# Performance work log

Measured on AMD Instinct MI355X. Metric: run time of the kernel, lower is better.

The kernel has to match this reference:

```python
import jax, jax.numpy as jnp
import numpy as np

B, S, D, H, FF = 4, 2048, 512, 8, 2048
HD = D // H
SCALE = float(D) ** 0.5  # original scales by sqrt(embed_dim), not sqrt(head_dim)
EPS = 1e-5


def setup_inputs() -> dict:
    key = jax.random.key(0)
    ks = jax.random.split(key, 16)
    s_in = 1.0 / np.sqrt(D)
    s_ff = 1.0 / np.sqrt(FF)
    return {
        "embeddings": jax.random.normal(ks[0], (B, S, D), dtype=jnp.float32),
        "mask": jnp.ones((B, S), dtype=bool),
        # per-head Q/K/V projections stacked: [H, D, HD]
        "Wq": jax.random.uniform(ks[1], (H, D, HD), jnp.float32, -s_in, s_in),
        "bq": jax.random.uniform(ks[2], (H, HD), jnp.float32, -s_in, s_in),
        "Wk": jax.random.uniform(ks[3], (H, D, HD), jnp.float32, -s_in, s_in),
        "bk": jax.random.uniform(ks[4], (H, HD), jnp.float32, -s_in, s_in),
        "Wv": jax.random.uniform(ks[5], (H, D, HD), jnp.float32, -s_in, s_in),
        "bv": jax.random.uniform(ks[6], (H, HD), jnp.float32, -s_in, s_in),
        "Wc": jax.random.uniform(ks[7], (D, D), jnp.float32, -s_in, s_in),
        "bc": jax.random.uniform(ks[8], (D,), jnp.float32, -s_in, s_in),
        "W1": jax.random.uniform(ks[9], (D, FF), jnp.float32, -s_in, s_in),
        "b1": jax.random.uniform(ks[10], (FF,), jnp.float32, -s_in, s_in),
        "W2": jax.random.uniform(ks[11], (FF, D), jnp.float32, -s_ff, s_ff),
        "b2": jax.random.uniform(ks[12], (D,), jnp.float32, -s_ff, s_ff),
        "gamma": jnp.ones((D,), jnp.float32),
        "beta": jnp.zeros((D,), jnp.float32),
    }


def reference(embeddings, mask, Wq, bq, Wk, bk, Wv, bv, Wc, bc, W1, b1, W2, b2, gamma, beta):
    # Per-head projections batched into one einsum each: [B,H,S,HD]
    Q = jnp.einsum("bsd,hdf->bhsf", embeddings, Wq) + bq[:, None, :]
    K = jnp.einsum("bsd,hdf->bhsf", embeddings, Wk) + bk[:, None, :]
    V = jnp.einsum("bsd,hdf->bhsf", embeddings, Wv) + bv[:, None, :]
    # NOTE: the original computes a masked score tensor but then softmaxes the
    # UNMASKED scores (bug). We faithfully ignore the mask here.
    scores = jnp.einsum("bhsf,bhtf->bhst", Q, K) / SCALE  # [B,H,S,S]
    A = jax.nn.softmax(scores, axis=-1)
    Hh = jnp.einsum("bhst,bhtf->bhsf", A, V)  # [B,H,S,HD]
    # concat heads along feature dim (head h -> contiguous slice)
    Hcat = jnp.transpose(Hh, (0, 2, 1, 3)).reshape(B, S, D)
    Hp = Hcat @ Wc + bc
    # add & norm (dropout is identity at eval)
    res = Hp + embeddings
    mu = jnp.mean(res, axis=-1, keepdims=True)
    var = jnp.var(res, axis=-1, keepdims=True)
    Hn = (res - mu) / jnp.sqrt(var + EPS) * gamma + beta
    out = jax.nn.relu(Hn @ W1 + b1) @ W2 + b2  # no residual after FFN in original
    return out, mask
```

## Files before the change

kernel.cpp:

```cpp
#include <hip/hip_runtime.h>
#include <hip/hip_bf16.h>
#include <cstdint>
#include <cstddef>

typedef short  s16x8 __attribute__((ext_vector_type(8)));
typedef short  s16x4 __attribute__((ext_vector_type(4)));
typedef float  f32x4 __attribute__((ext_vector_type(4)));
typedef unsigned u32x2 __attribute__((ext_vector_type(2)));

static constexpr int Bb = 4, Ss = 2048, Dd = 512, Hh = 8, HDd = 64, FFf = 2048;
static constexpr int Mm = Bb * Ss;

__device__ __forceinline__ unsigned short f2bf(float f) {
  unsigned u = __float_as_uint(f);
  u += 0x7FFFu + ((u >> 16) & 1u);
  return (unsigned short)(u >> 16);
}

__device__ __forceinline__ unsigned cvt_pk_bf16(float lo, float hi) {
  unsigned r;
  asm("v_cvt_pk_bf16_f32 %0, %1, %2" : "=v"(r) : "v"(lo), "v"(hi));
  return r;
}

__device__ __forceinline__ float exp2_raw(float x) {
  float r;
  asm("v_exp_f32 %0, %1\n\ts_nop 0" : "=v"(r) : "v"(x));
  return r;
}

#define GLOAD_LDS16(gp, lp)                                                     \
  __builtin_amdgcn_global_load_lds((const __attribute__((address_space(1))) void*)(gp), \
                                   (__attribute__((address_space(3))) void*)(lp), 16, 0, 0)

__device__ __forceinline__ void xpose_tile(const float* __restrict__ in,
                                           unsigned short* __restrict__ out,
                                           int K, int N, int bx, int by, float (*t)[33]) {
  const int lx = threadIdx.x & 31, ly = threadIdx.x >> 5;
  const int n0 = bx * 32, k0 = by * 32;
#pragma unroll
  for (int r = 0; r < 4; ++r) t[ly + r * 8][lx] = in[(size_t)(k0 + ly + r * 8) * N + n0 + lx];
  __syncthreads();
#pragma unroll
  for (int r = 0; r < 4; ++r)
    out[(size_t)(n0 + ly + r * 8) * K + k0 + lx] = f2bf(t[lx][ly + r * 8]);
}

__global__ __launch_bounds__(256) void prep_all(
    const float* __restrict__ emb, const float* __restrict__ Wq, const float* __restrict__ Wk,
    const float* __restrict__ Wv, const float* __restrict__ Wc, const float* __restrict__ W1,
    const float* __restrict__ W2, unsigned short* __restrict__ embB,
    unsigned short* __restrict__ WtQKV, unsigned short* __restrict__ WtC,
    unsigned short* __restrict__ Wt1, unsigned short* __restrict__ Wt2,
    float* __restrict__ maskOut) {
  __shared__ float t[32][33];
  const int blk = blockIdx.x;
  if (blk < 4096) {
    const int i = blk * 256 + threadIdx.x;
    const float4 v = reinterpret_cast<const float4*>(emb)[i];
    s16x4 o; o[0] = f2bf(v.x); o[1] = f2bf(v.y); o[2] = f2bf(v.z); o[3] = f2bf(v.w);
    reinterpret_cast<s16x4*>(embB)[i] = o;
  } else if (blk < 4864) {
    const int b = blk - 4096;
    const int bx = b & 15, by = (b >> 4) & 1, z = b >> 5;
    const int sel = z >> 3, h = z & 7;
    const float* W = sel == 0 ? Wq : (sel == 1 ? Wk : Wv);
    const float* inb = W + (size_t)h * 512 * 64;
    unsigned short* outb = WtQKV + (size_t)sel * 512 * 512 + (size_t)h * 64 * 512;
    const int lx = threadIdx.x & 31, ly = threadIdx.x >> 5;
    const int d0 = bx * 32, f0 = by * 32;
#pragma unroll
    for (int r = 0; r < 4; ++r) t[ly + r * 8][lx] = inb[(size_t)(d0 + ly + r * 8) * 64 + f0 + lx];
    __syncthreads();
#pragma unroll
    for (int r = 0; r < 4; ++r)
      outb[(size_t)(f0 + ly + r * 8) * 512 + d0 + lx] = f2bf(t[lx][ly + r * 8]);
  } else if (blk < 5120) {
    const int b = blk - 4864;
    xpose_tile(Wc, WtC, 512, 512, b & 15, b >> 4, t);
  } else if (blk < 6144) {
    const int b = blk - 5120;
    xpose_tile(W1, Wt1, 512, 2048, b & 63, b >> 6, t);
  } else if (blk < 7168) {
    const int b = blk - 6144;
    xpose_tile(W2, Wt2, 2048, 512, b & 15, b >> 4, t);
  } else {
    const int i = (blk - 7168) * 256 + threadIdx.x;
    if (i < Bb * Ss) maskOut[i] = 1.0f;
  }
}

template<int EPI, int NI>
__global__ __launch_bounds__(256) void gemm_bt(
    const unsigned short* __restrict__ A, const unsigned short* __restrict__ Bt,
    const float* __restrict__ bias0, const float* __restrict__ bias1, const float* __restrict__ bias2,
    const float* __restrict__ addf, float* __restrict__ outF,
    unsigned short* __restrict__ outB0, unsigned short* __restrict__ outB1,
    unsigned short* __restrict__ outB2, int M, int N, int K, int nbx) {
  constexpr int BN = NI * 32;
  __shared__ alignas(16) unsigned short As[3][128 * 32];
  __shared__ alignas(16) unsigned short Bs[3][BN * 32];
  const int tid = threadIdx.x;
  const int lane = tid & 63, wid = tid >> 6;
  const int wr = wid >> 1, wc = wid & 1;
  const int fr = lane & 15, kg = lane >> 4;

  const int lin = blockIdx.x;
  const int xcd = lin & 7, idx = lin >> 3;
  const int bx = idx % nbx, ysub = idx / nbx;
  const int m0 = (xcd * 8 + ysub) * 128, n0 = bx * BN;

  const int srow = tid >> 2;
  const int schunk = (tid & 3) ^ ((tid >> 3) & 3);
  const unsigned short* gA = A + (size_t)(m0 + srow) * K + (schunk << 3);
  const unsigned short* gB = Bt + (size_t)(n0 + srow) * K + (schunk << 3);

  auto STAGE = [&](int kt, int buf) {
    unsigned short* lA = &As[buf][wid * 512];
    unsigned short* lB = &Bs[buf][wid * 512];
    GLOAD_LDS16(gA + kt, lA);
    GLOAD_LDS16(gA + (size_t)64 * K + kt, lA + 2048);
    GLOAD_LDS16(gB + kt, lB);
    if constexpr (NI == 4) GLOAD_LDS16(gB + (size_t)64 * K + kt, lB + 2048);
  };

  f32x4 acc[4][NI];
#pragma unroll
  for (int i = 0; i < 4; ++i)
#pragma unroll
    for (int j = 0; j < NI; ++j)
#pragma unroll
      for (int r = 0; r < 4; ++r) acc[i][j][r] = 0.f;

  STAGE(0, 0);
  STAGE(32, 1);
  const int nk = K >> 5;
  int cur = 0;
  const int rchunk = (kg ^ ((fr >> 1) & 3)) << 3;
  for (int ki = 0; ki < nk; ++ki) {
    const int pre = cur == 0 ? 2 : cur - 1;
    __builtin_amdgcn_s_barrier();
    if (ki + 2 < nk) {
      STAGE((ki + 2) << 5, pre);
      if constexpr (NI == 4)
        asm volatile("s_waitcnt vmcnt(8)" ::: "memory");
      else
        asm volatile("s_waitcnt vmcnt(6)" ::: "memory");
    } else if (ki + 1 < nk) {
      if constexpr (NI == 4)
        asm volatile("s_waitcnt vmcnt(4)" ::: "memory");
      else
        asm volatile("s_waitcnt vmcnt(3)" ::: "memory");
    } else {
      asm volatile("s_waitcnt vmcnt(0)" ::: "memory");
    }
    __builtin_amdgcn_sched_barrier(0);
    __builtin_amdgcn_s_barrier();
    __builtin_amdgcn_sched_barrier(0);

    s16x8 af[4], bfv[NI];
#pragma unroll
    for (int i = 0; i < 4; ++i)
      af[i] = *reinterpret_cast<const s16x8*>(&As[cur][(wr * 64 + i * 16 + fr) * 32 + rchunk]);
#pragma unroll
    for (int i = 0; i < NI; ++i)
      bfv[i] = *reinterpret_cast<const s16x8*>(
          &Bs[cur][(wc * (NI * 16) + i * 16 + fr) * 32 + rchunk]);
    __builtin_amdgcn_s_setprio(1);
#pragma unroll
    for (int mi = 0; mi < 4; ++mi)
#pragma unroll
      for (int ni = 0; ni < NI; ++ni)
        acc[mi][ni] = __builtin_amdgcn_mfma_f32_16x16x32_bf16(af[mi], bfv[ni], acc[mi][ni], 0, 0, 0);
    __builtin_amdgcn_s_setprio(0);
    cur = cur == 2 ? 0 : cur + 1;
  }

#pragma unroll
  for (int mi = 0; mi < 4; ++mi)
#pragma unroll
    for (int ni = 0; ni < NI; ++ni) {
      if constexpr (EPI == 0) {
        const int col = n0 + wc * (NI * 16) + ni * 16 + fr;
        const int sel = col >> 9, c = col & 511;
        const int h = c >> 6, f = c & 63;
        const int row0 = m0 + wr * 64 + mi * 16 + kg * 4;
        const int b = row0 >> 11, s0 = row0 & 2047;
        if (sel == 2) {
          const float bsv = bias2[c];
          u32x2 pk;
          pk[0] = (unsigned)f2bf(acc[mi][ni][0] + bsv) |
                  ((unsigned)f2bf(acc[mi][ni][1] + bsv) << 16);
          pk[1] = (unsigned)f2bf(acc[mi][ni][2] + bsv) |
                  ((unsigned)f2bf(acc[mi][ni][3] + bsv) << 16);
          *reinterpret_cast<u32x2*>(
              &outB2[((size_t)((b << 3) + h) * 64 + f) * 2048 + s0]) = pk;
        } else {
          const float* bs = sel == 0 ? bias0 : bias1;
          unsigned short* ob = sel == 0 ? outB0 : outB1;
          const float bv = bs[c];
#pragma unroll
          for (int r = 0; r < 4; ++r)
            ob[((size_t)((b << 3) + h) * 2048 + s0 + r) * 64 + f] =
                f2bf(acc[mi][ni][r] + bv);
        }
      } else {
#pragma unroll
        for (int r = 0; r < 4; ++r) {
          const int row = m0 + wr * 64 + mi * 16 + kg * 4 + r;
          const int col = n0 + wc * (NI * 16) + ni * 16 + fr;
          float v = acc[mi][ni][r];
          if constexpr (EPI == 1) {
            const size_t idx2 = (size_t)row * 512 + col;
            outF[idx2] = v + bias0[col] + addf[idx2];
          } else if constexpr (EPI == 2) {
            v += bias0[col];
            outB0[(size_t)row * 2048 + col] = f2bf(v > 0.f ? v : 0.f);
          } else {
            outF[(size_t)row * 512 + col] = v + bias0[col];
          }
        }
      }
    }
}

__global__ __launch_bounds__(512) void attn_kernel(const unsigned short* __restrict__ Q,
                                                   const unsigned short* __restrict__ Kx,
                                                   const unsigned short* __restrict__ V,
                                                   unsigned short* __restrict__ Hcat) {
  const int lane = threadIdx.x & 63, wid = threadIdx.x >> 6;
  const int fr = lane & 15, kg = lane >> 4;
  const int lin = blockIdx.x;
  const int xcd = lin & 7, idx = lin >> 3;
  const int bh = xcd * 4 + (idx & 3);
  const int qi = idx >> 2;
  const int b = bh >> 3, h = bh & 7;
  const int q0 = qi * 128 + wid * 16;
  const unsigned short* Qh = Q + (size_t)bh * Ss * HDd;
  const unsigned short* Kh = Kx + (size_t)bh * Ss * HDd;
  const unsigned short* Vh = V + (size_t)bh * HDd * Ss;

  __shared__ alignas(16) unsigned short Ks[2][64 * 64];
  __shared__ alignas(16) unsigned short Vs[64 * 64];
  __shared__ alignas(16) unsigned short P[8][16][72];

  const int srow = lane >> 3;
  const int scol = ((lane & 7) ^ srow) << 3;
  const unsigned short* gK = Kh + (size_t)(8 * wid + srow) * 64 + scol;
  const unsigned short* gV = Vh + (size_t)(8 * wid + srow) * 2048 + scol;
  unsigned short* lKa = &Ks[0][wid * 512];
  unsigned short* lKb = &Ks[1][wid * 512];
  unsigned short* lV  = &Vs[wid * 512];

  s16x8 bq[2];
#pragma unroll
  for (int kb = 0; kb < 2; ++kb)
    bq[kb] = *reinterpret_cast<const s16x8*>(&Qh[(size_t)(q0 + fr) * 64 + kb * 32 + kg * 8]);

  f32x4 o[4];
#pragma unroll
  for (int ct = 0; ct < 4; ++ct)
#pragma unroll
    for (int r = 0; r < 4; ++r) o[ct][r] = 0.f;
  float mr = -1e30f, lsum = 0.f;

  const float iscL = 1.4426950408889634f * 0.044194173824159216f;
  const int swz = (fr & 7) << 3;

  GLOAD_LDS16(gK, lKa);
  GLOAD_LDS16(gV, lV);

#pragma unroll 1
  for (int t = 0; t < 32; ++t) {
    const int kt = t * 64;
    const int ktn = (kt + 64) & 2047;
    const unsigned short* KsC = Ks[t & 1];
    unsigned short* nK = (t & 1) ? lKa : lKb;

    asm volatile("s_waitcnt vmcnt(1)" ::: "memory");
    __builtin_amdgcn_sched_barrier(0);
    __builtin_amdgcn_s_barrier();
    __builtin_amdgcn_sched_barrier(0);

    f32x4 sc[4];
#pragma unroll
    for (int ct = 0; ct < 4; ++ct)
#pragma unroll
      for (int r = 0; r < 4; ++r) sc[ct][r] = 0.f;
    __builtin_amdgcn_s_setprio(1);
#pragma unroll
    for (int ct = 0; ct < 4; ++ct)
#pragma unroll
      for (int kb = 0; kb < 2; ++kb) {
        const s16x8 kf = *reinterpret_cast<const s16x8*>(
            &KsC[(ct * 16 + fr) * 64 + (((kg << 3) + (kb << 5)) ^ swz)]);
        sc[ct] = __builtin_amdgcn_mfma_f32_16x16x32_bf16(kf, bq[kb], sc[ct], 0, 0, 0);
      }
    __builtin_amdgcn_s_setprio(0);

    GLOAD_LDS16(gK + (size_t)ktn * 64, nK);

    float mxl;
    {
      const float a0 = fmaxf(fmaxf(sc[0][0], sc[0][1]), fmaxf(sc[0][2], sc[0][3]));
      const float a1 = fmaxf(fmaxf(sc[1][0], sc[1][1]), fmaxf(sc[1][2], sc[1][3]));
      const float a2 = fmaxf(fmaxf(sc[2][0], sc[2][1]), fmaxf(sc[2][2], sc[2][3]));
      const float a3 = fmaxf(fmaxf(sc[3][0], sc[3][1]), fmaxf(sc[3][2], sc[3][3]));
      mxl = fmaxf(fmaxf(a0, a1), fmaxf(a2, a3)) * iscL;
    }
    if (!__all(mxl <= mr + 8.0f)) {
      float mx = fmaxf(mxl, __shfl_xor(mxl, 16));
      mx = fmaxf(mx, __shfl_xor(mx, 32));
      const float mn = fmaxf(mr, mx);
      const float corr = exp2_raw(mr - mn);
      mr = mn;
      lsum *= corr;
      float corrq[4];
#pragma unroll
      for (int r = 0; r < 4; ++r) corrq[r] = __shfl(corr, kg * 4 + r);
#pragma unroll
      for (int ct = 0; ct < 4; ++ct)
#pragma unroll
        for (int r = 0; r < 4; ++r) o[ct][r] *= corrq[r];
    }

    float ps0 = 0.f, ps1 = 0.f;
#pragma unroll
    for (int ct = 0; ct < 4; ++ct) {
      float p0 = exp2_raw(__builtin_fmaf(sc[ct][0], iscL, -mr));
      float p1 = exp2_raw(__builtin_fmaf(sc[ct][1], iscL, -mr));
      float p2 = exp2_raw(__builtin_fmaf(sc[ct][2], iscL, -mr));
      float p3 = exp2_raw(__builtin_fmaf(sc[ct][3], iscL, -mr));
      ps0 += (p0 + p1);
      ps1 += (p2 + p3);
      u32x2 pk;
      pk[0] = cvt_pk_bf16(p0, p1);
      pk[1] = cvt_pk_bf16(p2, p3);
      *reinterpret_cast<u32x2*>(&P[wid][fr][ct * 16 + kg * 4]) = pk;
    }
    lsum += ps0 + ps1;

    asm volatile("s_waitcnt vmcnt(1)" ::: "memory");
    __builtin_amdgcn_sched_barrier(0);
    __builtin_amdgcn_s_barrier();
    __builtin_amdgcn_sched_barrier(0);

    const s16x8 pa0 = *reinterpret_cast<const s16x8*>(&P[wid][fr][kg * 8]);
    const s16x8 pa1 = *reinterpret_cast<const s16x8*>(&P[wid][fr][32 + kg * 8]);
    __builtin_amdgcn_s_setprio(1);
#pragma unroll
    for (int ct = 0; ct < 4; ++ct) {
      const s16x8 bv0 = *reinterpret_cast<const s16x8*>(
          &Vs[(ct * 16 + fr) * 64 + (((kg << 3) + 0) ^ swz)]);
      o[ct] = __builtin_amdgcn_mfma_f32_16x16x32_bf16(pa0, bv0, o[ct], 0, 0, 0);
      const s16x8 bv1 = *reinterpret_cast<const s16x8*>(
          &Vs[(ct * 16 + fr) * 64 + (((kg << 3) + 32) ^ swz)]);
      o[ct] = __builtin_amdgcn_mfma_f32_16x16x32_bf16(pa1, bv1, o[ct], 0, 0, 0);
    }
    __builtin_amdgcn_s_setprio(0);

    __builtin_amdgcn_s_barrier();
    __builtin_amdgcn_sched_barrier(0);
    GLOAD_LDS16(gV + ktn, lV);
  }

  lsum += __shfl_xor(lsum, 16);
  lsum += __shfl_xor(lsum, 32);
  float invq[4];
#pragma unroll
  for (int r = 0; r < 4; ++r) invq[r] = 1.0f / __shfl(lsum, kg * 4 + r);
#pragma unroll
  for (int ct = 0; ct < 4; ++ct)
#pragma unroll
    for (int r = 0; r < 4; ++r) {
      const int qrow = q0 + kg * 4 + r;
      Hcat[(size_t)(b * Ss + qrow) * Dd + h * 64 + ct * 16 + fr] = f2bf(o[ct][r] * invq[r]);
    }
}

__global__ __launch_bounds__(256) void layernorm_k(const float* __restrict__ res,
                                                   const float* __restrict__ gamma,
                                                   const float* __restrict__ beta,
                                                   unsigned short* __restrict__ out) {
  const int lane = threadIdx.x & 63, wid = threadIdx.x >> 6;
  const int row = blockIdx.x * 4 + wid;
  const float* rp = res + (size_t)row * 512 + lane * 8;
  const float4 v0 = *reinterpret_cast<const float4*>(rp);
  const float4 v1 = *reinterpret_cast<const float4*>(rp + 4);
  float x[8] = {v0.x, v0.y, v0.z, v0.w, v1.x, v1.y, v1.z, v1.w};
  float s = 0.f, q = 0.f;
#pragma unroll
  for (int j = 0; j < 8; ++j) { s += x[j]; q += x[j] * x[j]; }
#pragma unroll
  for (int off = 32; off; off >>= 1) { s += __shfl_xor(s, off); q += __shfl_xor(q, off); }
  const float mean = s * (1.f / 512.f);
  const float var = q * (1.f / 512.f) - mean * mean;
  const float rstd = rsqrtf(var + 1e-5f);
  s16x8 o;
#pragma unroll
  for (int j = 0; j < 8; ++j) {
    const int c = lane * 8 + j;
    o[j] = f2bf((x[j] - mean) * rstd * gamma[c] + beta[c]);
  }
  *reinterpret_cast<s16x8*>(out + (size_t)row * 512 + lane * 8) = o;
}

extern "C" void kernel_launch(void* const* d_in, const int* in_sizes, int n_in,
                              void* d_out, int out_size, void* d_ws, size_t ws_size,
                              hipStream_t stream) {
  const float* emb = (const float*)d_in[0];
  const float* Wq = (const float*)d_in[2];
  const float* bq = (const float*)d_in[3];
  const float* Wk = (const float*)d_in[4];
  const float* bk = (const float*)d_in[5];
  const float* Wv = (const float*)d_in[6];
  const float* bv = (const float*)d_in[7];
  const float* Wc = (const float*)d_in[8];
  const float* bc = (const float*)d_in[9];
  const float* W1 = (const float*)d_in[10];
  const float* b1 = (const float*)d_in[11];
  const float* W2 = (const float*)d_in[12];
  const float* b2 = (const float*)d_in[13];
  const float* gamma = (const float*)d_in[14];
  const float* beta = (const float*)d_in[15];
  float* out = (float*)d_out;

  char* ws = (char*)d_ws;
  size_t off = 0;
  auto alloc = [&](size_t bytes) {
    char* p = ws + off;
    off = (off + bytes + 255) & ~(size_t)255;
    return p;
  };
  unsigned short* embB = (unsigned short*)alloc((size_t)Mm * Dd * 2);
  unsigned short* WtQKV = (unsigned short*)alloc((size_t)1536 * 512 * 2);
  unsigned short* WtC = (unsigned short*)alloc((size_t)512 * 512 * 2);
  unsigned short* Wt1 = (unsigned short*)alloc((size_t)2048 * 512 * 2);
  unsigned short* Wt2 = (unsigned short*)alloc((size_t)512 * 2048 * 2);
  unsigned short* Qb = (unsigned short*)alloc((size_t)Mm * Dd * 2);
  unsigned short* Kb = (unsigned short*)alloc((size_t)Mm * Dd * 2);
  unsigned short* Vt = (unsigned short*)alloc((size_t)Mm * Dd * 2);
  unsigned short* Hcat = (unsigned short*)alloc((size_t)Mm * Dd * 2);
  float* resF = (float*)alloc((size_t)Mm * Dd * 4);
  unsigned short* HnB = (unsigned short*)alloc((size_t)Mm * Dd * 2);
  unsigned short* G = Qb;

  prep_all<<<7200, 256, 0, stream>>>(emb, Wq, Wk, Wv, Wc, W1, W2,
                                     embB, WtQKV, WtC, Wt1, Wt2,
                                     out + (size_t)Mm * Dd);

  gemm_bt<0, 4><<<768, 256, 0, stream>>>(embB, WtQKV, bq, bk, bv, nullptr, nullptr,
                                         Qb, Kb, Vt, Mm, 1536, 512, 12);
  attn_kernel<<<512, 512, 0, stream>>>(Qb, Kb, Vt, Hcat);
  gemm_bt<1, 2><<<512, 256, 0, stream>>>(Hcat, WtC, bc, nullptr, nullptr, emb, resF,
                                         nullptr, nullptr, nullptr, Mm, 512, 512, 8);
  layernorm_k<<<2048, 256, 0, stream>>>(resF, gamma, beta, HnB);
  gemm_bt<2, 4><<<1024, 256, 0, stream>>>(HnB, Wt1, b1, nullptr, nullptr, nullptr, nullptr,
                                          G, nullptr, nullptr, Mm, 2048, 512, 16);
  gemm_bt<3, 2><<<512, 256, 0, stream>>>(G, Wt2, b2, nullptr, nullptr, nullptr, out,
                                         nullptr, nullptr, nullptr, Mm, 512, 2048, 8);
}
```

Measured before the change: 166.3 us.

## Double attention KV tile to 128 keys per iteration and halve barriers

The attention loop now processes 128 keys per iteration instead of 64, with K double-buffered at 128 rows and V staged as a 64x128 tile with a new swizzle. The loop runs 16 times instead of 32, so barrier, wait and online-softmax rescale overhead is paid half as often. The K prefetch is issued right after the first barrier, and PV is done in two halves that reuse the per-wave P buffer. The launch bounds now request 4 blocks per CU. The costs are more LDS (about 66KB per block, which likely limits occupancy), more score registers, and a risk that the occupancy hint forces register spills.

```diff
diff --git a/kernel.cpp b/kernel.cpp
--- a/kernel.cpp
+++ b/kernel.cpp
@@ -224,10 +224,10 @@
     }
 }
 
-__global__ __launch_bounds__(512) void attn_kernel(const unsigned short* __restrict__ Q,
-                                                   const unsigned short* __restrict__ Kx,
-                                                   const unsigned short* __restrict__ V,
-                                                   unsigned short* __restrict__ Hcat) {
+__global__ __launch_bounds__(512, 4) void attn_kernel(const unsigned short* __restrict__ Q,
+                                                      const unsigned short* __restrict__ Kx,
+                                                      const unsigned short* __restrict__ V,
+                                                      unsigned short* __restrict__ Hcat) {
   const int lane = threadIdx.x & 63, wid = threadIdx.x >> 6;
   const int fr = lane & 15, kg = lane >> 4;
   const int lin = blockIdx.x;
@@ -240,17 +240,25 @@
   const unsigned short* Kh = Kx + (size_t)bh * Ss * HDd;
   const unsigned short* Vh = V + (size_t)bh * HDd * Ss;
 
-  __shared__ alignas(16) unsigned short Ks[2][64 * 64];
-  __shared__ alignas(16) unsigned short Vs[64 * 64];
+  __shared__ alignas(16) unsigned short Ks[2][128 * 64];
+  __shared__ alignas(16) unsigned short Vs[64 * 128];
   __shared__ alignas(16) unsigned short P[8][16][72];
 
   const int srow = lane >> 3;
-  const int scol = ((lane & 7) ^ srow) << 3;
-  const unsigned short* gK = Kh + (size_t)(8 * wid + srow) * 64 + scol;
-  const unsigned short* gV = Vh + (size_t)(8 * wid + srow) * 2048 + scol;
-  unsigned short* lKa = &Ks[0][wid * 512];
-  unsigned short* lKb = &Ks[1][wid * 512];
-  unsigned short* lV  = &Vs[wid * 512];
+  const int scolK = ((lane & 7) ^ srow) << 3;
+  const unsigned short* gK0 = Kh + (size_t)(8 * wid + srow) * 64 + scolK;
+  const unsigned short* gK1 = Kh + (size_t)(64 + 8 * wid + srow) * 64 + scolK;
+  unsigned short* lK0a = &Ks[0][wid * 512];
+  unsigned short* lK1a = &Ks[0][4096 + wid * 512];
+  unsigned short* lK0b = &Ks[1][wid * 512];
+  unsigned short* lK1b = &Ks[1][4096 + wid * 512];
+
+  const int vrow = wid * 4 + (lane >> 4);
+  const int scolV = ((lane & 15) ^ (vrow & 7)) << 3;
+  const unsigned short* gV0 = Vh + (size_t)vrow * 2048 + scolV;
+  const unsigned short* gV1 = Vh + (size_t)(32 + vrow) * 2048 + scolV;
+  unsigned short* lV0 = &Vs[wid * 512];
+  unsigned short* lV1 = &Vs[4096 + wid * 512];
 
   s16x8 bq[2];
 #pragma unroll
@@ -267,46 +275,51 @@
   const float iscL = 1.4426950408889634f * 0.044194173824159216f;
   const int swz = (fr & 7) << 3;
 
-  GLOAD_LDS16(gK, lKa);
-  GLOAD_LDS16(gV, lV);
+  GLOAD_LDS16(gK0, lK0a);
+  GLOAD_LDS16(gK1, lK1a);
+  GLOAD_LDS16(gV0, lV0);
+  GLOAD_LDS16(gV1, lV1);
 
 #pragma unroll 1
-  for (int t = 0; t < 32; ++t) {
-    const int kt = t * 64;
-    const int ktn = (kt + 64) & 2047;
+  for (int t = 0; t < 16; ++t) {
+    const int ktn = (t * 128 + 128) & 2047;
     const unsigned short* KsC = Ks[t & 1];
-    unsigned short* nK = (t & 1) ? lKa : lKb;
-
-    asm volatile("s_waitcnt vmcnt(1)" ::: "memory");
+    unsigned short* nK0 = (t & 1) ? lK0a : lK0b;
+    unsigned short* nK1 = (t & 1) ? lK1a : lK1b;
+
+    asm volatile("s_waitcnt vmcnt(2)" ::: "memory");
     __builtin_amdgcn_sched_barrier(0);
     __builtin_amdgcn_s_barrier();
     __builtin_amdgcn_sched_barrier(0);
 
-    f32x4 sc[4];
-#pragma unroll
-    for (int ct = 0; ct < 4; ++ct)
-#pragma unroll
-      for (int r = 0; r < 4; ++r) sc[ct][r] = 0.f;
+    GLOAD_LDS16(gK0 + (size_t)ktn * 64, nK0);
+    GLOAD_LDS16(gK1 + (size_t)ktn * 64, nK1);
+
+    f32x4 sc[8];
+#pragma unroll
+    for (int ctg = 0; ctg < 8; ++ctg)
+#pragma unroll
+      for (int r = 0; r < 4; ++r) sc[ctg][r] = 0.f;
     __builtin_amdgcn_s_setprio(1);
 #pragma unroll
-    for (int ct = 0; ct < 4; ++ct)
+    for (int ctg = 0; ctg < 8; ++ctg)
 #pragma unroll
       for (int kb = 0; kb < 2; ++kb) {
         const s16x8 kf = *reinterpret_cast<const s16x8*>(
-            &KsC[(ct * 16 + fr) * 64 + (((kg << 3) + (kb << 5)) ^ swz)]);
-        sc[ct] = __builtin_amdgcn_mfma_f32_16x16x32_bf16(kf, bq[kb], sc[ct], 0, 0, 0);
+            &KsC[(ctg * 16 + fr) * 64 + (((kg << 3) + (kb << 5)) ^ swz)]);
+        sc[ctg] = __builtin_amdgcn_mfma_f32_16x16x32_bf16(kf, bq[kb], sc[ctg], 0, 0, 0);
       }
     __builtin_amdgcn_s_setprio(0);
 
-    GLOAD_LDS16(gK + (size_t)ktn * 64, nK);
-
     float mxl;
     {
-      const float a0 = fmaxf(fmaxf(sc[0][0], sc[0][1]), fmaxf(sc[0][2], sc[0][3]));
-      const float a1 = fmaxf(fmaxf(sc[1][0], sc[1][1]), fmaxf(sc[1][2], sc[1][3]));
-      const float a2 = fmaxf(fmaxf(sc[2][0], sc[2][1]), fmaxf(sc[2][2], sc[2][3]));
-      const float a3 = fmaxf(fmaxf(sc[3][0], sc[3][1]), fmaxf(sc[3][2], sc[3][3]));
-      mxl = fmaxf(fmaxf(a0, a1), fmaxf(a2, a3)) * iscL;
+      float a[8];
+#pragma unroll
+      for (int ctg = 0; ctg < 8; ++ctg)
+        a[ctg] = fmaxf(fmaxf(sc[ctg][0], sc[ctg][1]), fmaxf(sc[ctg][2], sc[ctg][3]));
+      const float b0 = fmaxf(fmaxf(a[0], a[1]), fmaxf(a[2], a[3]));
+      const float b1 = fmaxf(fmaxf(a[4], a[5]), fmaxf(a[6], a[7]));
+      mxl = fmaxf(b0, b1) * iscL;
     }
     if (!__all(mxl <= mr + 8.0f)) {
       float mx = fmaxf(mxl, __shfl_xor(mxl, 16));
@@ -324,44 +337,49 @@
         for (int r = 0; r < 4; ++r) o[ct][r] *= corrq[r];
     }
 
-    float ps0 = 0.f, ps1 = 0.f;
-#pragma unroll
-    for (int ct = 0; ct < 4; ++ct) {
-      float p0 = exp2_raw(__builtin_fmaf(sc[ct][0], iscL, -mr));
-      float p1 = exp2_raw(__builtin_fmaf(sc[ct][1], iscL, -mr));
-      float p2 = exp2_raw(__builtin_fmaf(sc[ct][2], iscL, -mr));
-      float p3 = exp2_raw(__builtin_fmaf(sc[ct][3], iscL, -mr));
-      ps0 += (p0 + p1);
-      ps1 += (p2 + p3);
-      u32x2 pk;
-      pk[0] = cvt_pk_bf16(p0, p1);
-      pk[1] = cvt_pk_bf16(p2, p3);
-      *reinterpret_cast<u32x2*>(&P[wid][fr][ct * 16 + kg * 4]) = pk;
-    }
-    lsum += ps0 + ps1;
-
-    asm volatile("s_waitcnt vmcnt(1)" ::: "memory");
+    asm volatile("s_waitcnt vmcnt(2)" ::: "memory");
     __builtin_amdgcn_sched_barrier(0);
     __builtin_amdgcn_s_barrier();
     __builtin_amdgcn_sched_barrier(0);
 
-    const s16x8 pa0 = *reinterpret_cast<const s16x8*>(&P[wid][fr][kg * 8]);
-    const s16x8 pa1 = *reinterpret_cast<const s16x8*>(&P[wid][fr][32 + kg * 8]);
-    __builtin_amdgcn_s_setprio(1);
-#pragma unroll
-    for (int ct = 0; ct < 4; ++ct) {
-      const s16x8 bv0 = *reinterpret_cast<const s16x8*>(
-          &Vs[(ct * 16 + fr) * 64 + (((kg << 3) + 0) ^ swz)]);
-      o[ct] = __builtin_amdgcn_mfma_f32_16x16x32_bf16(pa0, bv0, o[ct], 0, 0, 0);
-      const s16x8 bv1 = *reinterpret_cast<const s16x8*>(
-          &Vs[(ct * 16 + fr) * 64 + (((kg << 3) + 32) ^ swz)]);
-      o[ct] = __builtin_amdgcn_mfma_f32_16x16x32_bf16(pa1, bv1, o[ct], 0, 0, 0);
-    }
-    __builtin_amdgcn_s_setprio(0);
+#pragma unroll
+    for (int half = 0; half < 2; ++half) {
+      float ps0 = 0.f, ps1 = 0.f;
+#pragma unroll
+      for (int ctl = 0; ctl < 4; ++ctl) {
+        const int ctg = half * 4 + ctl;
+        float p0 = exp2_raw(__builtin_fmaf(sc[ctg][0], iscL, -mr));
+        float p1 = exp2_raw(__builtin_fmaf(sc[ctg][1], iscL, -mr));
+        float p2 = exp2_raw(__builtin_fmaf(sc[ctg][2], iscL, -mr));
+        float p3 = exp2_raw(__builtin_fmaf(sc[ctg][3], iscL, -mr));
+        ps0 += (p0 + p1);
+        ps1 += (p2 + p3);
+        u32x2 pk;
+        pk[0] = cvt_pk_bf16(p0, p1);
+        pk[1] = cvt_pk_bf16(p2, p3);
+        *reinterpret_cast<u32x2*>(&P[wid][fr][ctl * 16 + kg * 4]) = pk;
+      }
+      lsum += ps0 + ps1;
+
+      const s16x8 pa0 = *reinterpret_cast<const s16x8*>(&P[wid][fr][kg * 8]);
+      const s16x8 pa1 = *reinterpret_cast<const s16x8*>(&P[wid][fr][32 + kg * 8]);
+      __builtin_amdgcn_s_setprio(1);
+#pragma unroll
+      for (int ct = 0; ct < 4; ++ct) {
+        const s16x8 bv0 = *reinterpret_cast<const s16x8*>(
+            &Vs[(ct * 16 + fr) * 128 + ((half * 64 + kg * 8) ^ swz)]);
+        o[ct] = __builtin_amdgcn_mfma_f32_16x16x32_bf16(pa0, bv0, o[ct], 0, 0, 0);
+        const s16x8 bv1 = *reinterpret_cast<const s16x8*>(
+            &Vs[(ct * 16 + fr) * 128 + ((half * 64 + 32 + kg * 8) ^ swz)]);
+        o[ct] = __builtin_amdgcn_mfma_f32_16x16x32_bf16(pa1, bv1, o[ct], 0, 0, 0);
+      }
+      __builtin_amdgcn_s_setprio(0);
+    }
 
     __builtin_amdgcn_s_barrier();
     __builtin_amdgcn_sched_barrier(0);
-    GLOAD_LDS16(gV + ktn, lV);
+    GLOAD_LDS16(gV0 + ktn, lV0);
+    GLOAD_LDS16(gV1 + ktn, lV1);
   }
 
   lsum += __shfl_xor(lsum, 16);
```

New measurement: 170.5 us. 2.5% more time.
